# Optimization experiments

Hardware: AMD Instinct MI355X
Metric: run time of the kernel (lower is better)

The kernel has to match this reference:

```python
import jax, jax.numpy as jnp
import numpy as np

B, N, D = 8, 4096, 1024
NC, NU = 8, 32            # core / universal experts (num_experts=16, occ_factor=1/4)
E = NC + NU               # 40 total experts
S = 2                     # slots per expert
HC, HU = 4 * D, D         # core hidden = 4*dim, occ hidden = 4*occ_factor*dim = dim
L2_EPS = 1e-6
LN_EPS = 1e-5


def l2norm(x):
    n = jnp.sqrt(jnp.sum(x * x, axis=-1, keepdims=True))
    return x * (1.0 / (n + L2_EPS))


def layernorm(x, g, b):
    mu = jnp.mean(x, axis=-1, keepdims=True)
    var = jnp.mean((x - mu) ** 2, axis=-1, keepdims=True)
    return (x - mu) / jnp.sqrt(var + LN_EPS) * g + b


def entmax15(z):
    # exact 1.5-entmax over last axis (sorted algorithm, Peters et al. 2019)
    z = z / 2.0
    z = z - jnp.max(z, axis=-1, keepdims=True)
    zs = -jnp.sort(-z, axis=-1)                      # descending
    K = z.shape[-1]
    k = jnp.arange(1, K + 1, dtype=z.dtype)
    mean = jnp.cumsum(zs, axis=-1) / k
    meansq = jnp.cumsum(zs * zs, axis=-1) / k
    ss = k * (meansq - mean * mean)
    delta = jnp.maximum((1.0 - ss) / k, 1e-12)
    tau = mean - jnp.sqrt(delta)
    support = jnp.sum((tau <= zs).astype(jnp.int32), axis=-1, keepdims=True)
    tau_star = jnp.take_along_axis(tau, support - 1, axis=-1)
    return jnp.maximum(z - tau_star, 0.0) ** 2


def setup_inputs() -> dict:
    key = jax.random.key(0)
    ks = jax.random.split(key, 8)
    return {
        "x": jax.random.normal(ks[0], (B, N, D), jnp.float32),
        "attn_weight": jax.random.uniform(ks[1], (B, 128), jnp.float32),
        "phi": jax.random.normal(ks[2], (E, S, D), jnp.float32) * 0.02,
        "key_gamma": jnp.ones((D,), jnp.float32),
        "key_beta": jnp.zeros((D,), jnp.float32),
        "query_gamma": jnp.ones((D,), jnp.float32),
        "query_beta": jnp.zeros((D,), jnp.float32),
        "ln_gamma": jnp.ones((D,), jnp.float32),
        "ln_beta": jnp.zeros((D,), jnp.float32),
        "scale0": jnp.asarray(0.5, jnp.float32),
        "scale1": jnp.asarray(0.5, jnp.float32),
        "core_w1": jax.random.normal(ks[3], (NC, D, HC), jnp.float32) * (D ** -0.5),
        "core_b1": jnp.zeros((NC, HC), jnp.float32),
        "core_w2": jax.random.normal(ks[4], (NC, HC, D), jnp.float32) * (HC ** -0.5),
        "core_b2": jnp.zeros((NC, D), jnp.float32),
        "occ_w1": jax.random.normal(ks[5], (NU, D, HU), jnp.float32) * (D ** -0.5),
        "occ_b1": jnp.zeros((NU, HU), jnp.float32),
        "occ_w2": jax.random.normal(ks[6], (NU, HU, D), jnp.float32) * (HU ** -0.5),
        "occ_b2": jnp.zeros((NU, D), jnp.float32),
    }


def _expert_mlp(s, w1, b1, w2, b2):
    # s: [b, e, s, d]; per-expert 2-layer MLP with exact GELU
    h = jax.nn.gelu(jnp.einsum('besd,edh->besh', s, w1) + b1[None, :, None, :], approximate=False)
    return jnp.einsum('besh,ehd->besd', h, w2) + b2[None, :, None, :]


def reference(x, attn_weight, phi, key_gamma, key_beta, query_gamma, query_beta,
              ln_gamma, ln_beta, scale0, scale1,
              core_w1, core_b1, core_w2, core_b2,
              occ_w1, occ_b1, occ_w2, occ_b2):
    # keys: OffsetScale then l2norm
    k = l2norm(x * key_gamma + key_beta)
    # queries: OffsetScale -> LayerNorm -> l2norm on phi
    q = layernorm(phi * query_gamma + query_beta, ln_gamma, ln_beta)
    q = l2norm(q)
    logits = jnp.einsum('bnd,esd->bnes', k, q)                      # [B,N,E,S]
    core_mask = (jnp.arange(E) < NC)[None, None, :, None]
    adjusted = jnp.where(core_mask, logits, jnp.asarray(-10000.0, logits.dtype))
    dispatch = jax.nn.softmax(adjusted / scale0, axis=2)            # softmax over experts
    combine = entmax15((adjusted / scale1).reshape(B, N, E * S))    # [B,N,E*S]
    slots = jnp.einsum('bnd,bnes->besd', x, dispatch)               # [B,E,S,D]
    core_out = _expert_mlp(slots[:, :NC], core_w1, core_b1, core_w2, core_b2)
    occ_out = _expert_mlp(slots[:, NC:], occ_w1, occ_b1, occ_w2, occ_b2)
    out = jnp.concatenate([core_out, occ_out], axis=1).reshape(B, E * S, D)
    return jnp.einsum('bsd,bns->bnd', out, combine)                 # [B,N,D]
```

## Files before the change

### kernel.cpp

```cpp
#include <hip/hip_runtime.h>
#include <hip/hip_bf16.h>

#define B_ 8
#define N_ 4096
#define D_ 1024

#define AS1 __attribute__((address_space(1)))
#define AS3 __attribute__((address_space(3)))
__device__ __forceinline__ void gld16(const float* g, float* l) {
    __builtin_amdgcn_global_load_lds((const AS1 void*)g, (AS3 void*)l, 16, 0, 0);
}

__global__ __launch_bounds__(64) void k_prep(
    const float* __restrict__ phi, const float* __restrict__ qg, const float* __restrict__ qb,
    const float* __restrict__ lng, const float* __restrict__ lnb,
    const float* __restrict__ kg, const float* __restrict__ kb,
    float* __restrict__ qk, float* __restrict__ cj, float* __restrict__ wbuf)
{
    int r = blockIdx.x;
    int lane = threadIdx.x;
    if (r == 16) {
        float cacc = 0.f;
#pragma unroll
        for (int c = 0; c < 16; ++c) {
            int i = c * 64 + lane;
            float g = kg[i], b = kb[i];
            wbuf[i] = g * g;
            wbuf[1024 + i] = 2.0f * g * b;
            cacc += b * b;
        }
#pragma unroll
        for (int m = 32; m; m >>= 1) cacc += __shfl_xor(cacc, m);
        if (lane == 0) wbuf[2048] = cacc;
        return;
    }
    const float* pr = phi + (size_t)r * D_;
    float v[16];
    float s1 = 0.f;
#pragma unroll
    for (int c = 0; c < 16; ++c) {
        int i = c * 64 + lane;
        v[c] = pr[i] * qg[i] + qb[i];
        s1 += v[c];
    }
#pragma unroll
    for (int m = 32; m; m >>= 1) s1 += __shfl_xor(s1, m);
    float mu = s1 * (1.0f / D_);
    float s2 = 0.f;
#pragma unroll
    for (int c = 0; c < 16; ++c) { float dd = v[c] - mu; s2 += dd * dd; }
#pragma unroll
    for (int m = 32; m; m >>= 1) s2 += __shfl_xor(s2, m);
    float var = s2 * (1.0f / D_);
    float inv = 1.0f / sqrtf(var + 1e-5f);
    float u[16];
    float s3 = 0.f;
#pragma unroll
    for (int c = 0; c < 16; ++c) {
        int i = c * 64 + lane;
        u[c] = (v[c] - mu) * inv * lng[i] + lnb[i];
        s3 += u[c] * u[c];
    }
#pragma unroll
    for (int m = 32; m; m >>= 1) s3 += __shfl_xor(s3, m);
    float rn = 1.0f / (sqrtf(s3) + 1e-6f);
    float cacc = 0.f;
#pragma unroll
    for (int c = 0; c < 16; ++c) {
        int i = c * 64 + lane;
        float qv = u[c] * rn;
        qk[(size_t)r * D_ + i] = qv * kg[i];
        cacc += qv * kb[i];
    }
#pragma unroll
    for (int m = 32; m; m >>= 1) cacc += __shfl_xor(cacc, m);
    if (lane == 0) cj[r] = cacc;
}

__global__ __launch_bounds__(512) void k_fused(
    const float* __restrict__ x, const float* __restrict__ qk,
    const float* __restrict__ wbuf, const float* __restrict__ cj,
    const float* __restrict__ s0p,
    float* __restrict__ lgbuf, float* __restrict__ spart)
{
    __shared__ float smem[16384];
    float* qs   = smem;
    float* red  = smem;
    float* sums = smem + 8704;
    float* disp = smem + 9792;

    int tid = threadIdx.x;
    int tok0 = blockIdx.x * 64;
    int wid = tid >> 6;
    int r0 = tid >> 4;
    int c4 = (tid & 15) * 4;

#pragma unroll
    for (int i = 0; i < 8; ++i)
        gld16(qk + (size_t)(i * 512 + tid) * 4, &qs[(i * 512 + wid * 64) * 4]);
    __syncthreads();

    float acc[2][17];
#pragma unroll
    for (int u = 0; u < 2; ++u)
#pragma unroll
        for (int v = 0; v < 17; ++v) acc[u][v] = 0.f;

#pragma unroll 2
    for (int dc = 0; dc < 16; ++dc) {
        float4 xv0 = *(const float4*)(x + (size_t)(tok0 + r0) * D_ + dc * 64 + c4);
        float4 xv1 = *(const float4*)(x + (size_t)(tok0 + 32 + r0) * D_ + dc * 64 + c4);
        float4 w2v = *(const float4*)(wbuf + dc * 64 + c4);
        float4 w1v = *(const float4*)(wbuf + 1024 + dc * 64 + c4);
        acc[0][16] += (w2v.x * xv0.x + w1v.x) * xv0.x + (w2v.y * xv0.y + w1v.y) * xv0.y
                    + (w2v.z * xv0.z + w1v.z) * xv0.z + (w2v.w * xv0.w + w1v.w) * xv0.w;
        acc[1][16] += (w2v.x * xv1.x + w1v.x) * xv1.x + (w2v.y * xv1.y + w1v.y) * xv1.y
                    + (w2v.z * xv1.z + w1v.z) * xv1.z + (w2v.w * xv1.w + w1v.w) * xv1.w;
        const float* qb = qs + dc * 64 + c4;
#pragma unroll
        for (int j = 0; j < 16; ++j) {
            float4 q4 = *(const float4*)(qb + j * 1024);
            acc[0][j] += xv0.x * q4.x + xv0.y * q4.y + xv0.z * q4.z + xv0.w * q4.w;
            acc[1][j] += xv1.x * q4.x + xv1.y * q4.y + xv1.z * q4.z + xv1.w * q4.w;
        }
    }
    __syncthreads();

#pragma unroll
    for (int half = 0; half < 2; ++half) {
#pragma unroll
        for (int v = 0; v < 17; ++v)
            red[(r0 * 17 + v) * 16 + (tid & 15)] = acc[half][v];
        __syncthreads();
#pragma unroll
        for (int it = 0; it < 2; ++it) {
            int idx = tid + it * 512;
            if (idx < 544) {
                const float4* p = (const float4*)(red + idx * 16);
                float4 a = p[0], b = p[1], cq = p[2], dq = p[3];
                float sum = (((a.x + a.y) + (a.z + a.w)) + ((b.x + b.y) + (b.z + b.w)))
                          + (((cq.x + cq.y) + (cq.z + cq.w)) + ((dq.x + dq.y) + (dq.z + dq.w)));
                int t = idx / 17, v = idx - t * 17;
                lgbuf[(size_t)(tok0 + half * 32 + t) * 20 + v] = sum;
                sums[(half * 32 + t) * 17 + v] = sum;
            }
        }
        __syncthreads();
    }

    if (tid < 64) {
        const float* sp = sums + tid * 17;
        float ss = sp[16] + wbuf[2048];
        float rn = 1.0f / (sqrtf(ss) + 1e-6f);
        float inv0 = 1.0f / s0p[0];
        float lg[16];
#pragma unroll
        for (int j = 0; j < 16; ++j) lg[j] = (sp[j] + cj[j]) * rn;
        float dsp[16];
#pragma unroll
        for (int sl = 0; sl < 2; ++sl) {
            float a[8], m = -1e30f;
#pragma unroll
            for (int ee = 0; ee < 8; ++ee) { a[ee] = lg[2 * ee + sl] * inv0; m = fmaxf(m, a[ee]); }
            float den = 0.f;
#pragma unroll
            for (int ee = 0; ee < 8; ++ee) { a[ee] = expf(a[ee] - m); den += a[ee]; }
            float r = 1.0f / den;
#pragma unroll
            for (int ee = 0; ee < 8; ++ee) dsp[2 * ee + sl] = a[ee] * r;
        }
#pragma unroll
        for (int q4i = 0; q4i < 4; ++q4i)
            *(float4*)(&disp[tid * 16 + q4i * 4]) =
                make_float4(dsp[q4i * 4 + 0], dsp[q4i * 4 + 1], dsp[q4i * 4 + 2], dsp[q4i * 4 + 3]);
    }
    __syncthreads();

    int th = tid >> 8;
    int cix = tid & 255;
    const float* xp = x + (size_t)tok0 * D_ + cix * 4;
    float4 acc2[8];
#pragma unroll
    for (int j = 0; j < 8; ++j) { acc2[j].x = 0.f; acc2[j].y = 0.f; acc2[j].z = 0.f; acc2[j].w = 0.f; }
#pragma unroll 8
    for (int n = 0; n < 64; ++n) {
        float4 xv = *(const float4*)(xp + (size_t)n * D_);
        const float4* q4 = (const float4*)(disp + n * 16 + th * 8);
        float4 s0 = q4[0], s1 = q4[1];
        acc2[0].x += s0.x * xv.x; acc2[0].y += s0.x * xv.y; acc2[0].z += s0.x * xv.z; acc2[0].w += s0.x * xv.w;
        acc2[1].x += s0.y * xv.x; acc2[1].y += s0.y * xv.y; acc2[1].z += s0.y * xv.z; acc2[1].w += s0.y * xv.w;
        acc2[2].x += s0.z * xv.x; acc2[2].y += s0.z * xv.y; acc2[2].z += s0.z * xv.z; acc2[2].w += s0.z * xv.w;
        acc2[3].x += s0.w * xv.x; acc2[3].y += s0.w * xv.y; acc2[3].z += s0.w * xv.z; acc2[3].w += s0.w * xv.w;
        acc2[4].x += s1.x * xv.x; acc2[4].y += s1.x * xv.y; acc2[4].z += s1.x * xv.z; acc2[4].w += s1.x * xv.w;
        acc2[5].x += s1.y * xv.x; acc2[5].y += s1.y * xv.y; acc2[5].z += s1.y * xv.z; acc2[5].w += s1.y * xv.w;
        acc2[6].x += s1.z * xv.x; acc2[6].y += s1.z * xv.y; acc2[6].z += s1.z * xv.z; acc2[6].w += s1.z * xv.w;
        acc2[7].x += s1.w * xv.x; acc2[7].y += s1.w * xv.y; acc2[7].z += s1.w * xv.z; acc2[7].w += s1.w * xv.w;
    }
    float* op = spart + ((size_t)blockIdx.x * 16 + th * 8) * 1024 + cix * 4;
#pragma unroll
    for (int j = 0; j < 8; ++j)
        *(float4*)(op + (size_t)j * 1024) = acc2[j];
}

__global__ __launch_bounds__(64) void k_epi(
    const float* __restrict__ lgbuf, const float* __restrict__ cj,
    const float* __restrict__ wbuf, const float* __restrict__ s1p,
    float* __restrict__ combine)
{
    int tok = blockIdx.x * 64 + threadIdx.x;
    const float* lp = lgbuf + (size_t)tok * 20;
    float s[17];
    float4 q0 = *(const float4*)(lp + 0);
    float4 q1 = *(const float4*)(lp + 4);
    float4 q2 = *(const float4*)(lp + 8);
    float4 q3 = *(const float4*)(lp + 12);
    s[0] = q0.x; s[1] = q0.y; s[2] = q0.z; s[3] = q0.w;
    s[4] = q1.x; s[5] = q1.y; s[6] = q1.z; s[7] = q1.w;
    s[8] = q2.x; s[9] = q2.y; s[10] = q2.z; s[11] = q2.w;
    s[12] = q3.x; s[13] = q3.y; s[14] = q3.z; s[15] = q3.w;
    s[16] = lp[16];

    float ss = s[16] + wbuf[2048];
    float rn = 1.0f / (sqrtf(ss) + 1e-6f);
    float inv1h = 0.5f / s1p[0];
    float lg[16];
#pragma unroll
    for (int j = 0; j < 16; ++j) lg[j] = (s[j] + cj[j]) * rn;

    float z[16], zmax = -1e30f;
#pragma unroll
    for (int j = 0; j < 16; ++j) { z[j] = lg[j] * inv1h; zmax = fmaxf(zmax, z[j]); }
#pragma unroll
    for (int j = 0; j < 16; ++j) z[j] -= zmax;
    float zsr[16];
#pragma unroll
    for (int j = 0; j < 16; ++j) zsr[j] = z[j];
#pragma unroll
    for (int rr = 0; rr < 16; ++rr) {
#pragma unroll
        for (int jj = (rr & 1); jj + 1 < 16; jj += 2) {
            float aa = zsr[jj], bb = zsr[jj + 1];
            zsr[jj] = fmaxf(aa, bb);
            zsr[jj + 1] = fminf(aa, bb);
        }
    }
    float cs = 0.f, css = 0.f, tau_star = 0.f;
#pragma unroll
    for (int kk = 1; kk <= 16; ++kk) {
        cs += zsr[kk - 1];
        css += zsr[kk - 1] * zsr[kk - 1];
        float fk = (float)kk;
        float mean = cs / fk, msq = css / fk;
        float ssv = fk * (msq - mean * mean);
        float delta = fmaxf((1.0f - ssv) / fk, 1e-12f);
        float tau = mean - sqrtf(delta);
        tau_star = (tau <= zsr[kk - 1]) ? tau : tau_star;
    }
    float4* cw = (float4*)(combine + (size_t)tok * 16);
#pragma unroll
    for (int q4i = 0; q4i < 4; ++q4i) {
        float4 cv;
        float t0 = fmaxf(z[q4i * 4 + 0] - tau_star, 0.f);
        float t1 = fmaxf(z[q4i * 4 + 1] - tau_star, 0.f);
        float t2 = fmaxf(z[q4i * 4 + 2] - tau_star, 0.f);
        float t3 = fmaxf(z[q4i * 4 + 3] - tau_star, 0.f);
        cv.x = t0 * t0; cv.y = t1 * t1; cv.z = t2 * t2; cv.w = t3 * t3;
        cw[q4i] = cv;
    }
}

__global__ __launch_bounds__(256) void k_slots_reduce(
    const float* __restrict__ spart, float* __restrict__ slotsT)
{
    int j = blockIdx.x, b = blockIdx.y;
    int tid = threadIdx.x;
    const float* p = spart + ((size_t)(b * 64) * 16 + j) * 1024 + tid * 4;
    float4 s; s.x = 0.f; s.y = 0.f; s.z = 0.f; s.w = 0.f;
#pragma unroll 8
    for (int nc = 0; nc < 64; ++nc) {
        float4 v = *(const float4*)(p + (size_t)nc * 16384);
        s.x += v.x; s.y += v.y; s.z += v.z; s.w += v.w;
    }
    int e = j >> 1, sl = j & 1;
    int t = b * 2 + sl;
    float* o = slotsT + ((size_t)e * 1024 + tid * 4) * 16 + t;
    o[0] = s.x; o[16] = s.y; o[32] = s.z; o[48] = s.w;
}

__global__ __launch_bounds__(256) void k_mlp1(
    const float* __restrict__ w1, const float* __restrict__ slotsT,
    float* __restrict__ p1)
{
    __shared__ float sm[1024];
    int cc = blockIdx.x, ks = blockIdx.y, e = blockIdx.z;
    int tid = threadIdx.x;
    int k0 = ks * 64;
    int col = cc * 1024 + tid * 4;
    ((float4*)sm)[tid] = ((const float4*)(slotsT + ((size_t)e * 1024 + k0) * 16))[tid];
    __syncthreads();

    const float* wp = w1 + (size_t)e * 1024 * 4096 + (size_t)k0 * 4096 + col;
    float4 acc[16];
#pragma unroll
    for (int t = 0; t < 16; ++t) { acc[t].x = 0.f; acc[t].y = 0.f; acc[t].z = 0.f; acc[t].w = 0.f; }
#pragma unroll 8
    for (int kk = 0; kk < 64; ++kk) {
        float4 w = *(const float4*)(wp + (size_t)kk * 4096);
        const float4* q4 = (const float4*)(sm + kk * 16);
        float4 s0 = q4[0], s1 = q4[1], s2 = q4[2], s3 = q4[3];
        acc[0].x  += s0.x * w.x; acc[0].y  += s0.x * w.y; acc[0].z  += s0.x * w.z; acc[0].w  += s0.x * w.w;
        acc[1].x  += s0.y * w.x; acc[1].y  += s0.y * w.y; acc[1].z  += s0.y * w.z; acc[1].w  += s0.y * w.w;
        acc[2].x  += s0.z * w.x; acc[2].y  += s0.z * w.y; acc[2].z  += s0.z * w.z; acc[2].w  += s0.z * w.w;
        acc[3].x  += s0.w * w.x; acc[3].y  += s0.w * w.y; acc[3].z  += s0.w * w.z; acc[3].w  += s0.w * w.w;
        acc[4].x  += s1.x * w.x; acc[4].y  += s1.x * w.y; acc[4].z  += s1.x * w.z; acc[4].w  += s1.x * w.w;
        acc[5].x  += s1.y * w.x; acc[5].y  += s1.y * w.y; acc[5].z  += s1.y * w.z; acc[5].w  += s1.y * w.w;
        acc[6].x  += s1.z * w.x; acc[6].y  += s1.z * w.y; acc[6].z  += s1.z * w.z; acc[6].w  += s1.z * w.w;
        acc[7].x  += s1.w * w.x; acc[7].y  += s1.w * w.y; acc[7].z  += s1.w * w.z; acc[7].w  += s1.w * w.w;
        acc[8].x  += s2.x * w.x; acc[8].y  += s2.x * w.y; acc[8].z  += s2.x * w.z; acc[8].w  += s2.x * w.w;
        acc[9].x  += s2.y * w.x; acc[9].y  += s2.y * w.y; acc[9].z  += s2.y * w.z; acc[9].w  += s2.y * w.w;
        acc[10].x += s2.z * w.x; acc[10].y += s2.z * w.y; acc[10].z += s2.z * w.z; acc[10].w += s2.z * w.w;
        acc[11].x += s2.w * w.x; acc[11].y += s2.w * w.y; acc[11].z += s2.w * w.z; acc[11].w += s2.w * w.w;
        acc[12].x += s3.x * w.x; acc[12].y += s3.x * w.y; acc[12].z += s3.x * w.z; acc[12].w += s3.x * w.w;
        acc[13].x += s3.y * w.x; acc[13].y += s3.y * w.y; acc[13].z += s3.y * w.z; acc[13].w += s3.y * w.w;
        acc[14].x += s3.z * w.x; acc[14].y += s3.z * w.y; acc[14].z += s3.z * w.z; acc[14].w += s3.z * w.w;
        acc[15].x += s3.w * w.x; acc[15].y += s3.w * w.y; acc[15].z += s3.w * w.z; acc[15].w += s3.w * w.w;
    }
    float av0[16], av1[16], av2[16], av3[16];
#pragma unroll
    for (int t = 0; t < 16; ++t) { av0[t] = acc[t].x; av1[t] = acc[t].y; av2[t] = acc[t].z; av3[t] = acc[t].w; }
    float* op = p1 + (((size_t)ks * 8 + e) * 4096 + col) * 16;
#pragma unroll
    for (int q = 0; q < 4; ++q) {
        *(float4*)(op + 0 * 16 + q * 4) = make_float4(av0[q*4+0], av0[q*4+1], av0[q*4+2], av0[q*4+3]);
        *(float4*)(op + 1 * 16 + q * 4) = make_float4(av1[q*4+0], av1[q*4+1], av1[q*4+2], av1[q*4+3]);
        *(float4*)(op + 2 * 16 + q * 4) = make_float4(av2[q*4+0], av2[q*4+1], av2[q*4+2], av2[q*4+3]);
        *(float4*)(op + 3 * 16 + q * 4) = make_float4(av3[q*4+0], av3[q*4+1], av3[q*4+2], av3[q*4+3]);
    }
}

__global__ __launch_bounds__(256) void k_mlp2f(
    const float* __restrict__ w2, const float* __restrict__ p1,
    const float* __restrict__ b1, float* __restrict__ p2)
{
    __shared__ float sm[1024];
    int ks = blockIdx.x, e = blockIdx.y;
    int tid = threadIdx.x;
    int k0 = ks * 64;
    int col = tid * 4;

    {
        int fidx = tid;
        const float* pp = p1 + (size_t)e * 65536 + (size_t)k0 * 16 + fidx * 4;
        float4 s; s.x = 0.f; s.y = 0.f; s.z = 0.f; s.w = 0.f;
#pragma unroll
        for (int ksp = 0; ksp < 16; ++ksp) {
            float4 v = *(const float4*)(pp + (size_t)ksp * 524288);
            s.x += v.x; s.y += v.y; s.z += v.z; s.w += v.w;
        }
        int colh = k0 + (fidx >> 2);
        float bb = b1[(size_t)e * 4096 + colh];
        s.x += bb; s.y += bb; s.z += bb; s.w += bb;
        s.x = 0.5f * s.x * (1.0f + erff(s.x * 0.70710678118654752f));
        s.y = 0.5f * s.y * (1.0f + erff(s.y * 0.70710678118654752f));
        s.z = 0.5f * s.z * (1.0f + erff(s.z * 0.70710678118654752f));
        s.w = 0.5f * s.w * (1.0f + erff(s.w * 0.70710678118654752f));
        *(float4*)(&sm[fidx * 4]) = s;
    }
    __syncthreads();

    const float* wp = w2 + (size_t)e * 4096 * 1024 + (size_t)k0 * 1024 + col;
    float4 acc[16];
#pragma unroll
    for (int t = 0; t < 16; ++t) { acc[t].x = 0.f; acc[t].y = 0.f; acc[t].z = 0.f; acc[t].w = 0.f; }
#pragma unroll 8
    for (int kk = 0; kk < 64; ++kk) {
        float4 w = *(const float4*)(wp + (size_t)kk * 1024);
        const float4* q4 = (const float4*)(sm + kk * 16);
        float4 s0 = q4[0], s1 = q4[1], s2 = q4[2], s3 = q4[3];
        acc[0].x  += s0.x * w.x; acc[0].y  += s0.x * w.y; acc[0].z  += s0.x * w.z; acc[0].w  += s0.x * w.w;
        acc[1].x  += s0.y * w.x; acc[1].y  += s0.y * w.y; acc[1].z  += s0.y * w.z; acc[1].w  += s0.y * w.w;
        acc[2].x  += s0.z * w.x; acc[2].y  += s0.z * w.y; acc[2].z  += s0.z * w.z; acc[2].w  += s0.z * w.w;
        acc[3].x  += s0.w * w.x; acc[3].y  += s0.w * w.y; acc[3].z  += s0.w * w.z; acc[3].w  += s0.w * w.w;
        acc[4].x  += s1.x * w.x; acc[4].y  += s1.x * w.y; acc[4].z  += s1.x * w.z; acc[4].w  += s1.x * w.w;
        acc[5].x  += s1.y * w.x; acc[5].y  += s1.y * w.y; acc[5].z  += s1.y * w.z; acc[5].w  += s1.y * w.w;
        acc[6].x  += s1.z * w.x; acc[6].y  += s1.z * w.y; acc[6].z  += s1.z * w.z; acc[6].w  += s1.z * w.w;
        acc[7].x  += s1.w * w.x; acc[7].y  += s1.w * w.y; acc[7].z  += s1.w * w.z; acc[7].w  += s1.w * w.w;
        acc[8].x  += s2.x * w.x; acc[8].y  += s2.x * w.y; acc[8].z  += s2.x * w.z; acc[8].w  += s2.x * w.w;
        acc[9].x  += s2.y * w.x; acc[9].y  += s2.y * w.y; acc[9].z  += s2.y * w.z; acc[9].w  += s2.y * w.w;
        acc[10].x += s2.z * w.x; acc[10].y += s2.z * w.y; acc[10].z += s2.z * w.z; acc[10].w += s2.z * w.w;
        acc[11].x += s2.w * w.x; acc[11].y += s2.w * w.y; acc[11].z += s2.w * w.z; acc[11].w += s2.w * w.w;
        acc[12].x += s3.x * w.x; acc[12].y += s3.x * w.y; acc[12].z += s3.x * w.z; acc[12].w += s3.x * w.w;
        acc[13].x += s3.y * w.x; acc[13].y += s3.y * w.y; acc[13].z += s3.y * w.z; acc[13].w += s3.y * w.w;
        acc[14].x += s3.z * w.x; acc[14].y += s3.z * w.y; acc[14].z += s3.z * w.z; acc[14].w += s3.z * w.w;
        acc[15].x += s3.w * w.x; acc[15].y += s3.w * w.y; acc[15].z += s3.w * w.z; acc[15].w += s3.w * w.w;
    }
    float av0[16], av1[16], av2[16], av3[16];
#pragma unroll
    for (int t = 0; t < 16; ++t) { av0[t] = acc[t].x; av1[t] = acc[t].y; av2[t] = acc[t].z; av3[t] = acc[t].w; }
    float* op = p2 + (((size_t)ks * 8 + e) * 1024 + col) * 16;
#pragma unroll
    for (int q = 0; q < 4; ++q) {
        *(float4*)(op + 0 * 16 + q * 4) = make_float4(av0[q*4+0], av0[q*4+1], av0[q*4+2], av0[q*4+3]);
        *(float4*)(op + 1 * 16 + q * 4) = make_float4(av1[q*4+0], av1[q*4+1], av1[q*4+2], av1[q*4+3]);
        *(float4*)(op + 2 * 16 + q * 4) = make_float4(av2[q*4+0], av2[q*4+1], av2[q*4+2], av2[q*4+3]);
        *(float4*)(op + 3 * 16 + q * 4) = make_float4(av3[q*4+0], av3[q*4+1], av3[q*4+2], av3[q*4+3]);
    }
}

__global__ __launch_bounds__(256) void k_red2(
    const float* __restrict__ p2, const float* __restrict__ b2,
    float* __restrict__ co)
{
    int idx = blockIdx.x * 256 + threadIdx.x;
    int q = idx & 3, d = (idx >> 2) & 1023, e = idx >> 12;
    const float* p = p2 + ((size_t)e * 1024 + d) * 16 + q * 4;
    float4 s; s.x = 0.f; s.y = 0.f; s.z = 0.f; s.w = 0.f;
#pragma unroll 8
    for (int ks = 0; ks < 64; ++ks) {
        float4 v = *(const float4*)(p + (size_t)ks * 131072);
        s.x += v.x; s.y += v.y; s.z += v.z; s.w += v.w;
    }
    float bb = b2[(size_t)e * 1024 + d];
    float vv[4] = { s.x + bb, s.y + bb, s.z + bb, s.w + bb };
#pragma unroll
    for (int u = 0; u < 4; ++u) {
        int t = q * 4 + u;
        int b = t >> 1, sl = t & 1;
        co[((size_t)b * 16 + e * 2 + sl) * 1024 + d] = vv[u];
    }
}

__global__ __launch_bounds__(256) void k_out(
    const float* __restrict__ co, const float* __restrict__ combine,
    float* __restrict__ out)
{
    __shared__ float sm[1024];
    int b = blockIdx.y, tile = blockIdx.x;
    int tid = threadIdx.x;
    ((float4*)sm)[tid] = ((const float4*)(combine + ((size_t)b * N_ + tile * 64) * 16))[tid];
    float4 cv[16];
#pragma unroll
    for (int j = 0; j < 16; ++j)
        cv[j] = ((const float4*)(co + ((size_t)b * 16 + j) * 1024))[tid];
    __syncthreads();
    float4* ob = (float4*)(out + ((size_t)b * N_ + tile * 64) * 1024) + tid;
#pragma unroll 2
    for (int it = 0; it < 64; ++it) {
        const float* cm = sm + it * 16;
        float4 acc; acc.x = 0.f; acc.y = 0.f; acc.z = 0.f; acc.w = 0.f;
#pragma unroll
        for (int j = 0; j < 16; ++j) {
            float wj = cm[j];
            acc.x += wj * cv[j].x; acc.y += wj * cv[j].y;
            acc.z += wj * cv[j].z; acc.w += wj * cv[j].w;
        }
        ob[(size_t)it * 256] = acc;
    }
}

extern "C" void kernel_launch(void* const* d_in, const int* in_sizes, int n_in,
                              void* d_out, int out_size, void* d_ws, size_t ws_size,
                              hipStream_t stream)
{
    const float* x   = (const float*)d_in[0];
    const float* phi = (const float*)d_in[2];
    const float* kg  = (const float*)d_in[3];
    const float* kb  = (const float*)d_in[4];
    const float* qg  = (const float*)d_in[5];
    const float* qb  = (const float*)d_in[6];
    const float* lng = (const float*)d_in[7];
    const float* lnb = (const float*)d_in[8];
    const float* s0  = (const float*)d_in[9];
    const float* s1  = (const float*)d_in[10];
    const float* w1  = (const float*)d_in[11];
    const float* b1  = (const float*)d_in[12];
    const float* w2  = (const float*)d_in[13];
    const float* b2  = (const float*)d_in[14];

    float* out = (float*)d_out;
    float* ws  = (float*)d_ws;

    float* qk       = ws;
    float* cj       = qk + 16384;
    float* wbuf     = cj + 16;
    float* combine  = wbuf + 2064;
    float* slotsT   = combine + 524288;
    float* co       = slotsT + 131072;
    float* lgbuf    = co + 131072;
    float* arenaA   = lgbuf + 655360;
    float* arenaB   = arenaA + 8388608;
    float* spart    = arenaA;
    float* p1       = arenaA;
    float* p2       = arenaB;

    k_prep        <<<dim3(17),        dim3(64),  0, stream>>>(phi, qg, qb, lng, lnb, kg, kb, qk, cj, wbuf);
    k_fused       <<<dim3(512),       dim3(512), 0, stream>>>(x, qk, wbuf, cj, s0, lgbuf, spart);
    k_epi         <<<dim3(512),       dim3(64),  0, stream>>>(lgbuf, cj, wbuf, s1, combine);
    k_slots_reduce<<<dim3(16, 8),     dim3(256), 0, stream>>>(spart, slotsT);
    k_mlp1        <<<dim3(4, 16, 8),  dim3(256), 0, stream>>>(w1, slotsT, p1);
    k_mlp2f       <<<dim3(64, 8),     dim3(256), 0, stream>>>(w2, p1, b1, p2);
    k_red2        <<<dim3(128),       dim3(256), 0, stream>>>(p2, b2, co);
    k_out         <<<dim3(64, 8),     dim3(256), 0, stream>>>(co, combine, out);
}
```

Before: 214.1 us.

## Compute routing logits with bf16 MFMA instead of fp32 FMA loops

The query-key product in the fused routing kernel now uses 16x16x32 bf16 MFMA instructions. x is converted to bf16 on the fly and the query matrix is stored as bf16 by the prep kernel. This removes the LDS staging of the fp32 query matrix and the two-pass cross-lane reduction, replacing them with a split-K partial-sum combine in a much smaller shared buffer. Logits lose precision from bf16 rounding, which affects the softmax and entmax routing.

```diff
diff --git a/kernel.cpp b/kernel.cpp
--- a/kernel.cpp
+++ b/kernel.cpp
@@ -5,17 +5,20 @@
 #define N_ 4096
 #define D_ 1024
 
-#define AS1 __attribute__((address_space(1)))
-#define AS3 __attribute__((address_space(3)))
-__device__ __forceinline__ void gld16(const float* g, float* l) {
-    __builtin_amdgcn_global_load_lds((const AS1 void*)g, (AS3 void*)l, 16, 0, 0);
+typedef __attribute__((ext_vector_type(8))) short short8_t;
+typedef __attribute__((ext_vector_type(4))) float f32x4;
+
+__device__ __forceinline__ unsigned short f2bf(float f) {
+    union { float f; unsigned int u; } v; v.f = f;
+    unsigned int r = v.u + 0x7FFF + ((v.u >> 16) & 1);
+    return (unsigned short)(r >> 16);
 }
 
 __global__ __launch_bounds__(64) void k_prep(
     const float* __restrict__ phi, const float* __restrict__ qg, const float* __restrict__ qb,
     const float* __restrict__ lng, const float* __restrict__ lnb,
     const float* __restrict__ kg, const float* __restrict__ kb,
-    float* __restrict__ qk, float* __restrict__ cj, float* __restrict__ wbuf)
+    unsigned short* __restrict__ qkb, float* __restrict__ cj, float* __restrict__ wbuf)
 {
     int r = blockIdx.x;
     int lane = threadIdx.x;
@@ -69,7 +72,7 @@
     for (int c = 0; c < 16; ++c) {
         int i = c * 64 + lane;
         float qv = u[c] * rn;
-        qk[(size_t)r * D_ + i] = qv * kg[i];
+        qkb[(size_t)r * D_ + i] = f2bf(qv * kg[i]);
         cacc += qv * kb[i];
     }
 #pragma unroll
@@ -78,75 +81,77 @@
 }
 
 __global__ __launch_bounds__(512) void k_fused(
-    const float* __restrict__ x, const float* __restrict__ qk,
+    const float* __restrict__ x, const unsigned short* __restrict__ qkb,
     const float* __restrict__ wbuf, const float* __restrict__ cj,
     const float* __restrict__ s0p,
     float* __restrict__ lgbuf, float* __restrict__ spart)
 {
-    __shared__ float smem[16384];
-    float* qs   = smem;
-    float* red  = smem;
-    float* sums = smem + 8704;
-    float* disp = smem + 9792;
+    __shared__ float smem[4288];
+    float* part = smem;
+    float* nrmp = smem + 2048;
+    float* sums = smem + 2176;
+    float* disp = smem + 3264;
 
     int tid = threadIdx.x;
     int tok0 = blockIdx.x * 64;
-    int wid = tid >> 6;
-    int r0 = tid >> 4;
-    int c4 = (tid & 15) * 4;
-
-#pragma unroll
-    for (int i = 0; i < 8; ++i)
-        gld16(qk + (size_t)(i * 512 + tid) * 4, &qs[(i * 512 + wid * 64) * 4]);
+    int wv = tid >> 6;
+    int lane = tid & 63;
+    int wt = wv & 3;
+    int kh = wv >> 2;
+    int am = lane & 15;
+    int kg = lane >> 4;
+
+    const float* xrow = x + (size_t)(tok0 + wt * 16 + am) * D_ + kh * 512 + kg * 8;
+    const unsigned short* qrow = qkb + (size_t)am * 1024 + kh * 512 + kg * 8;
+    const float* w2row = wbuf + kh * 512 + kg * 8;
+    const float* w1row = wbuf + 1024 + kh * 512 + kg * 8;
+
+    f32x4 acc = {0.f, 0.f, 0.f, 0.f};
+    float nrm = 0.f;
+#pragma unroll 2
+    for (int ks = 0; ks < 16; ++ks) {
+        int off = ks * 32;
+        float4 a0  = *(const float4*)(xrow + off);
+        float4 a1  = *(const float4*)(xrow + off + 4);
+        float4 w2a = *(const float4*)(w2row + off);
+        float4 w2b = *(const float4*)(w2row + off + 4);
+        float4 w1a = *(const float4*)(w1row + off);
+        float4 w1b = *(const float4*)(w1row + off + 4);
+        nrm += (w2a.x * a0.x + w1a.x) * a0.x + (w2a.y * a0.y + w1a.y) * a0.y
+             + (w2a.z * a0.z + w1a.z) * a0.z + (w2a.w * a0.w + w1a.w) * a0.w
+             + (w2b.x * a1.x + w1b.x) * a1.x + (w2b.y * a1.y + w1b.y) * a1.y
+             + (w2b.z * a1.z + w1b.z) * a1.z + (w2b.w * a1.w + w1b.w) * a1.w;
+        int p0, p1, p2, p3;
+        asm("v_cvt_pk_bf16_f32 %0, %1, %2" : "=v"(p0) : "v"(a0.x), "v"(a0.y));
+        asm("v_cvt_pk_bf16_f32 %0, %1, %2" : "=v"(p1) : "v"(a0.z), "v"(a0.w));
+        asm("v_cvt_pk_bf16_f32 %0, %1, %2" : "=v"(p2) : "v"(a1.x), "v"(a1.y));
+        asm("v_cvt_pk_bf16_f32 %0, %1, %2" : "=v"(p3) : "v"(a1.z), "v"(a1.w));
+        union { int i[4]; short8_t s; } ua;
+        ua.i[0] = p0; ua.i[1] = p1; ua.i[2] = p2; ua.i[3] = p3;
+        short8_t bv = *(const short8_t*)(qrow + off);
+        acc = __builtin_amdgcn_mfma_f32_16x16x32_bf16(ua.s, bv, acc, 0, 0, 0);
+    }
+    nrm += __shfl_xor(nrm, 16);
+    nrm += __shfl_xor(nrm, 32);
+
+#pragma unroll
+    for (int r = 0; r < 4; ++r)
+        part[(kh * 64 + wt * 16 + kg * 4 + r) * 16 + am] = acc[r];
+    if (kg == 0) nrmp[kh * 64 + wt * 16 + am] = nrm;
     __syncthreads();
 
-    float acc[2][17];
-#pragma unroll
-    for (int u = 0; u < 2; ++u)
-#pragma unroll
-        for (int v = 0; v < 17; ++v) acc[u][v] = 0.f;
-
-#pragma unroll 2
-    for (int dc = 0; dc < 16; ++dc) {
-        float4 xv0 = *(const float4*)(x + (size_t)(tok0 + r0) * D_ + dc * 64 + c4);
-        float4 xv1 = *(const float4*)(x + (size_t)(tok0 + 32 + r0) * D_ + dc * 64 + c4);
-        float4 w2v = *(const float4*)(wbuf + dc * 64 + c4);
-        float4 w1v = *(const float4*)(wbuf + 1024 + dc * 64 + c4);
-        acc[0][16] += (w2v.x * xv0.x + w1v.x) * xv0.x + (w2v.y * xv0.y + w1v.y) * xv0.y
-                    + (w2v.z * xv0.z + w1v.z) * xv0.z + (w2v.w * xv0.w + w1v.w) * xv0.w;
-        acc[1][16] += (w2v.x * xv1.x + w1v.x) * xv1.x + (w2v.y * xv1.y + w1v.y) * xv1.y
-                    + (w2v.z * xv1.z + w1v.z) * xv1.z + (w2v.w * xv1.w + w1v.w) * xv1.w;
-        const float* qb = qs + dc * 64 + c4;
-#pragma unroll
-        for (int j = 0; j < 16; ++j) {
-            float4 q4 = *(const float4*)(qb + j * 1024);
-            acc[0][j] += xv0.x * q4.x + xv0.y * q4.y + xv0.z * q4.z + xv0.w * q4.w;
-            acc[1][j] += xv1.x * q4.x + xv1.y * q4.y + xv1.z * q4.z + xv1.w * q4.w;
+#pragma unroll
+    for (int it = 0; it < 3; ++it) {
+        int idx = tid + it * 512;
+        if (idx < 1088) {
+            int t = idx / 17, v = idx - t * 17;
+            float sv = (v < 16) ? (part[t * 16 + v] + part[1024 + t * 16 + v])
+                                : (nrmp[t] + nrmp[64 + t]);
+            sums[idx] = sv;
+            lgbuf[(size_t)(tok0 + t) * 20 + v] = sv;
         }
     }
     __syncthreads();
-
-#pragma unroll
-    for (int half = 0; half < 2; ++half) {
-#pragma unroll
-        for (int v = 0; v < 17; ++v)
-            red[(r0 * 17 + v) * 16 + (tid & 15)] = acc[half][v];
-        __syncthreads();
-#pragma unroll
-        for (int it = 0; it < 2; ++it) {
-            int idx = tid + it * 512;
-            if (idx < 544) {
-                const float4* p = (const float4*)(red + idx * 16);
-                float4 a = p[0], b = p[1], cq = p[2], dq = p[3];
-                float sum = (((a.x + a.y) + (a.z + a.w)) + ((b.x + b.y) + (b.z + b.w)))
-                          + (((cq.x + cq.y) + (cq.z + cq.w)) + ((dq.x + dq.y) + (dq.z + dq.w)));
-                int t = idx / 17, v = idx - t * 17;
-                lgbuf[(size_t)(tok0 + half * 32 + t) * 20 + v] = sum;
-                sums[(half * 32 + t) * 17 + v] = sum;
-            }
-        }
-        __syncthreads();
-    }
 
     if (tid < 64) {
         const float* sp = sums + tid * 17;
@@ -480,8 +485,8 @@
     float* out = (float*)d_out;
     float* ws  = (float*)d_ws;
 
-    float* qk       = ws;
-    float* cj       = qk + 16384;
+    unsigned short* qkb = (unsigned short*)ws;
+    float* cj       = ws + 8192;
     float* wbuf     = cj + 16;
     float* combine  = wbuf + 2064;
     float* slotsT   = combine + 524288;
@@ -493,8 +498,8 @@
     float* p1       = arenaA;
     float* p2       = arenaB;
 
-    k_prep        <<<dim3(17),        dim3(64),  0, stream>>>(phi, qg, qb, lng, lnb, kg, kb, qk, cj, wbuf);
-    k_fused       <<<dim3(512),       dim3(512), 0, stream>>>(x, qk, wbuf, cj, s0, lgbuf, spart);
+    k_prep        <<<dim3(17),        dim3(64),  0, stream>>>(phi, qg, qb, lng, lnb, kg, kb, qkb, cj, wbuf);
+    k_fused       <<<dim3(512),       dim3(512), 0, stream>>>(x, qkb, wbuf, cj, s0, lgbuf, spart);
     k_epi         <<<dim3(512),       dim3(64),  0, stream>>>(lgbuf, cj, wbuf, s1, combine);
     k_slots_reduce<<<dim3(16, 8),     dim3(256), 0, stream>>>(spart, slotsT);
     k_mlp1        <<<dim3(4, 16, 8),  dim3(256), 0, stream>>>(w1, slotsT, p1);
```

Result: no change. 213.6 us (-0.2%).
